# Kernel tuning notes

Hardware: AMD Instinct MI355X
Metric: run time of the kernel (lower is better)

## Reference

```python
import jax, jax.numpy as jnp
import numpy as np

B, S, D, H, DK, DV = 4, 2048, 512, 8, 64, 64
LN_EPS = 1e-5


def setup_inputs() -> dict:
    key = jax.random.key(0)
    ks = jax.random.split(key, 8)
    scale = 1.0 / np.sqrt(D)
    return {
        "input_Q": jax.random.normal(ks[0], (B, S, D), jnp.float32),
        "input_K": jax.random.normal(ks[1], (B, S, D), jnp.float32),
        "input_V": jax.random.normal(ks[2], (B, S, D), jnp.float32),
        "attn_mask": jax.random.randint(ks[3], (B, S, S), 0, 2).astype(jnp.bool_),
        "W_Q": jax.random.normal(ks[4], (D, H * DK), jnp.float32) * scale,
        "W_K": jax.random.normal(ks[5], (D, H * DK), jnp.float32) * scale,
        "W_V": jax.random.normal(ks[6], (D, H * DV), jnp.float32) * scale,
        "W_fc": jax.random.normal(ks[7], (H * DV, D), jnp.float32) * scale,
        "ln_gamma": jnp.ones((D,), jnp.float32),
        "ln_beta": jnp.zeros((D,), jnp.float32),
    }


def reference(input_Q, input_K, input_V, attn_mask, W_Q, W_K, W_V, W_fc, ln_gamma, ln_beta):
    b, s, _ = input_Q.shape
    # projections -> [b, h, s, d]
    Q = (input_Q @ W_Q).reshape(b, s, H, DK).transpose(0, 2, 1, 3)
    K = (input_K @ W_K).reshape(b, s, H, DK).transpose(0, 2, 1, 3)
    V = (input_V @ W_V).reshape(b, s, H, DV).transpose(0, 2, 1, 3)
    # full [b, h, q, k] score matrix (faithful to explicit matmul->mask->softmax)
    scores = jnp.einsum("bhqd,bhkd->bhqk", Q, K) / np.sqrt(DK).astype(np.float32)
    scores = jnp.where(attn_mask[:, None, :, :], -jnp.inf, scores)
    attn = jax.nn.softmax(scores, axis=-1)
    context = jnp.einsum("bhqk,bhkd->bhqd", attn, V)  # [b, h, s, dv]
    context = context.transpose(0, 2, 1, 3).reshape(b, s, H * DV)
    output = context @ W_fc  # dropout is identity in eval / p=0
    x = output + input_Q  # residual
    mean = jnp.mean(x, axis=-1, keepdims=True)
    var = jnp.var(x, axis=-1, keepdims=True)
    return (x - mean) * jax.lax.rsqrt(var + LN_EPS) * ln_gamma + ln_beta
```

## Files before the change

### kernel.cpp

```cpp
#include <hip/hip_runtime.h>


#define B_ 4
#define S_ 2048
#define D_ 512
#define H_ 8

typedef __attribute__((ext_vector_type(8))) short short8_t;
typedef __attribute__((ext_vector_type(4))) short short4_t;
typedef __attribute__((ext_vector_type(4))) float f32x4;
typedef __attribute__((ext_vector_type(16))) float f32x16;
typedef __attribute__((ext_vector_type(4))) unsigned u32x4;
typedef __attribute__((ext_vector_type(2))) unsigned u32x2;

__device__ __forceinline__ short f2bf(float f) {
    unsigned u = __builtin_bit_cast(unsigned, f);
    u += 0x7fff + ((u >> 16) & 1);
    return (short)(u >> 16);
}

__device__ __forceinline__ unsigned pk2(float a, float b) {
    return __builtin_amdgcn_perm(__builtin_bit_cast(unsigned, b),
                                 __builtin_bit_cast(unsigned, a), 0x07060302u);
}

__device__ __forceinline__ float bflo(unsigned u) {
    return __builtin_bit_cast(float, u << 16);
}
__device__ __forceinline__ float bfhi(unsigned u) {
    return __builtin_bit_cast(float, u & 0xffff0000u);
}

__device__ __forceinline__ void gload16(const void* g, void* l) {
    __builtin_amdgcn_global_load_lds(
        (const __attribute__((address_space(1))) unsigned int*)g,
        (__attribute__((address_space(3))) unsigned int*)l, 16, 0, 0);
}

__global__ __launch_bounds__(256) void pack_mask_kernel(const void* __restrict__ mask,
                                                        unsigned* __restrict__ bits) {
    __shared__ int isBool;
    if (threadIdx.x == 0) isBool = 0;
    __syncthreads();
    const unsigned char* bytes = (const unsigned char*)mask;
    if (threadIdx.x < 64) {
        if (bytes[threadIdx.x * 4 + 1] | bytes[threadIdx.x * 4 + 2] | bytes[threadIdx.x * 4 + 3])
            isBool = 1;
    }
    __syncthreads();
    int w = blockIdx.x * 256 + threadIdx.x;
    size_t base = (size_t)w * 32;
    unsigned v = 0;
    if (isBool) {
        const unsigned char* p = bytes + base;
        #pragma unroll
        for (int i = 0; i < 32; ++i) v |= (p[i] ? 1u : 0u) << i;
    } else {
        const int* p = (const int*)mask + base;
        #pragma unroll
        for (int i = 0; i < 32; ++i) v |= (p[i] ? 1u : 0u) << i;
    }
    bits[w] = ~v;
}

__global__ __launch_bounds__(256) void proj_kernel(
    const float* __restrict__ inQ, const float* __restrict__ inK, const float* __restrict__ inV,
    const float* __restrict__ wq, const float* __restrict__ wk, const float* __restrict__ wv,
    short* __restrict__ Qp, short* __restrict__ Kp, short* __restrict__ Vp) {
    __shared__ short As[64 * 64];
    __shared__ short Bs[64 * 64];
    const int z = blockIdx.z;
    const float* A = (z == 0) ? inQ : ((z == 1) ? inK : inV);
    const float* W = (z == 0) ? wq : ((z == 1) ? wk : wv);
    short* O = (z == 0) ? Qp : ((z == 1) ? Kp : Vp);
    const float scale = (z == 0) ? 0.125f * 1.44269504f : 1.0f;
    const int bm = blockIdx.x * 64, bn = blockIdx.y * 64;
    const int tid = threadIdx.x, lane = tid & 63, wv_ = tid >> 6;
    const int wm = (wv_ >> 1) * 32, wn = (wv_ & 1) * 32;
    f32x4 acc[2][2] = {};

    for (int k0 = 0; k0 < 512; k0 += 64) {
        __syncthreads();
        #pragma unroll
        for (int it = 0; it < 4; ++it) {
            int g = tid + it * 256;
            int r = g >> 4, c4 = (g & 15) * 4;
            f32x4 v = *(const f32x4*)(A + (size_t)(bm + r) * 512 + k0 + c4);
            u32x2 u = { pk2(v.x, v.y), pk2(v.z, v.w) };
            *(u32x2*)((char*)As + r * 128 + ((c4 * 2) ^ ((r & 7) << 4))) = u;
        }
        #pragma unroll
        for (int it = 0; it < 2; ++it) {
            int g = tid + it * 256;
            int kp = g >> 4, n4 = (g & 15) * 4;
            const float* wrow = W + (size_t)(k0 + 2 * kp) * 512 + bn + n4;
            f32x4 va = *(const f32x4*)(wrow);
            f32x4 vb = *(const f32x4*)(wrow + 512);
            #pragma unroll
            for (int j = 0; j < 4; ++j) {
                int n = n4 + j;
                *(unsigned*)((char*)Bs + n * 128 + ((4 * kp) ^ ((n & 7) << 4))) = pk2(va[j], vb[j]);
            }
        }
        __syncthreads();
        #pragma unroll
        for (int kk = 0; kk < 2; ++kk) {
            short8_t af[2], bfr[2];
            #pragma unroll
            for (int rf = 0; rf < 2; ++rf) {
                int row = wm + rf * 16 + (lane & 15);
                af[rf] = *(const short8_t*)((const char*)As + row * 128 +
                          ((kk * 64 + ((lane >> 4) * 16)) ^ ((row & 7) << 4)));
            }
            #pragma unroll
            for (int cf = 0; cf < 2; ++cf) {
                int n = wn + cf * 16 + (lane & 15);
                bfr[cf] = *(const short8_t*)((const char*)Bs + n * 128 +
                           ((kk * 64 + ((lane >> 4) * 16)) ^ ((n & 7) << 4)));
            }
            __builtin_amdgcn_s_setprio(1);
            #pragma unroll
            for (int rf = 0; rf < 2; ++rf)
                #pragma unroll
                for (int cf = 0; cf < 2; ++cf)
                    acc[rf][cf] = __builtin_amdgcn_mfma_f32_16x16x32_bf16(af[rf], bfr[cf], acc[rf][cf], 0, 0, 0);
            __builtin_amdgcn_s_setprio(0);
        }
    }
    if (z == 2) {
        #pragma unroll
        for (int rf = 0; rf < 2; ++rf)
            #pragma unroll
            for (int cf = 0; cf < 2; ++cf) {
                int col = bn + wn + cf * 16 + (lane & 15);
                int row0 = bm + wm + rf * 16 + (lane >> 4) * 4;
                int bb = row0 >> 11, ss = row0 & 2047;
                size_t off = ((size_t)(bb * 8 + (col >> 6)) * 64 + (col & 63)) * 2048 + ss;
                short4_t v4 = { f2bf(acc[rf][cf][0]), f2bf(acc[rf][cf][1]),
                                f2bf(acc[rf][cf][2]), f2bf(acc[rf][cf][3]) };
                *(short4_t*)(O + off) = v4;
            }
    } else {
        #pragma unroll
        for (int rf = 0; rf < 2; ++rf)
            #pragma unroll
            for (int cf = 0; cf < 2; ++cf)
                #pragma unroll
                for (int r = 0; r < 4; ++r) {
                    int row = bm + wm + rf * 16 + (lane >> 4) * 4 + r;
                    int col = bn + wn + cf * 16 + (lane & 15);
                    size_t idx = ((((size_t)(row >> 11)) * 8 + (col >> 6)) * 2048 + (row & 2047)) * 64 + (col & 63);
                    O[idx] = f2bf(acc[rf][cf][r] * scale);
                }
    }
}

template<int NSPLIT>
__global__ __launch_bounds__(256, 4) void attn_kernel(
    const short* __restrict__ Qp, const short* __restrict__ Kp, const short* __restrict__ Vt,
    const unsigned long long* __restrict__ mbits64, short* __restrict__ ctx,
    short* __restrict__ pO, float* __restrict__ pL) {
    __shared__ short Ks[2][64 * 64];
    __shared__ short Vts[2][64 * 64];
    const int b = blockIdx.z;
    const int h = (NSPLIT > 1) ? ((int)blockIdx.y / NSPLIT) : blockIdx.y;
    const int kvh = (NSPLIT > 1) ? ((int)blockIdx.y % NSPLIT) : 0;
    const int q_blk = blockIdx.x * 128;
    const int tid = threadIdx.x, lane = tid & 63, w = tid >> 6;
    const int hi = lane >> 5, r31 = lane & 31;
    const size_t hb = ((size_t)(b * 8 + h)) * 131072;
    const int qw = q_blk + w * 32;
    const int q_lane = qw + r31;
    const int NT = 32 / NSPLIT;
    const int t_beg = kvh * NT;
    const int t_end = t_beg + NT;

    short8_t qf[4];
    #pragma unroll
    for (int ks = 0; ks < 4; ++ks)
        qf[ks] = *(const short8_t*)(Qp + hb + (size_t)q_lane * 64 + ks * 16 + hi * 8);

    f32x16 o0 = {}, o1 = {};
    float l_run = 0.f;

    const int sub = lane >> 3, chk = lane & 7;
    const int colsrc = (chk * 16) ^ (sub << 4);
    const int swz = (lane & 7) << 4;

    #pragma unroll
    for (int ii = 0; ii < 2; ++ii) {
        int row = w * 16 + ii * 8 + sub;
        gload16((const char*)(Kp + hb + (size_t)(t_beg * 64 + row) * 64) + colsrc, &Ks[0][(w * 16 + ii * 8) * 64]);
        gload16((const char*)(Vt + hb + (size_t)row * 2048 + t_beg * 64) + colsrc, &Vts[0][(w * 16 + ii * 8) * 64]);
    }
    __syncthreads();

    for (int kt = t_beg; kt < t_end; ++kt) {
        const int buf = (kt - t_beg) & 1;
        const short* Kb = Ks[buf];
        const short* Vb = Vts[buf];
        if (kt < t_end - 1) {
            int nb = buf ^ 1;
            #pragma unroll
            for (int ii = 0; ii < 2; ++ii) {
                int row = w * 16 + ii * 8 + sub;
                gload16((const char*)(Kp + hb + (size_t)((kt + 1) * 64 + row) * 64) + colsrc,
                        &Ks[nb][(w * 16 + ii * 8) * 64]);
                gload16((const char*)(Vt + hb + (size_t)row * 2048 + (kt + 1) * 64) + colsrc,
                        &Vts[nb][(w * 16 + ii * 8) * 64]);
            }
        }
        unsigned long long wmx = mbits64[((size_t)(b * 2048 + q_lane)) * 32 + kt] >> (hi * 4);
        unsigned kl = (unsigned)wmx, kh = (unsigned)(wmx >> 32);

        f32x16 s0 = {}, s1 = {};
        __builtin_amdgcn_s_setprio(1);
        #pragma unroll
        for (int ks = 0; ks < 4; ++ks) {
            short8_t kf0 = *(const short8_t*)((const char*)Kb + (size_t)r31 * 128 + ((ks * 32 + hi * 16) ^ swz));
            short8_t kf1 = *(const short8_t*)((const char*)Kb + (size_t)(32 + r31) * 128 + ((ks * 32 + hi * 16) ^ swz));
            s0 = __builtin_amdgcn_mfma_f32_32x32x16_bf16(kf0, qf[ks], s0, 0, 0, 0);
            s1 = __builtin_amdgcn_mfma_f32_32x32x16_bf16(kf1, qf[ks], s1, 0, 0, 0);
        }
        __builtin_amdgcn_s_setprio(0);

        float r4[4] = { 0.f, 0.f, 0.f, 0.f };
        #pragma unroll
        for (int reg = 0; reg < 16; ++reg) {
            const int pos = (reg >> 2) * 8 + (reg & 3);
            float e0 = __builtin_amdgcn_exp2f(s0[reg]);
            float e1 = __builtin_amdgcn_exp2f(s1[reg]);
            unsigned k0b = (unsigned)__builtin_amdgcn_sbfe((int)kl, pos, 1);
            unsigned k1b = (unsigned)__builtin_amdgcn_sbfe((int)kh, pos, 1);
            float v0 = __builtin_bit_cast(float, __builtin_bit_cast(unsigned, e0) & k0b);
            float v1 = __builtin_bit_cast(float, __builtin_bit_cast(unsigned, e1) & k1b);
            s0[reg] = v0; s1[reg] = v1;
            r4[reg & 3] += v0 + v1;
        }
        float rs = (r4[0] + r4[1]) + (r4[2] + r4[3]);
        rs += __shfl_xor(rs, 32, 64);
        l_run += rs;

        #pragma unroll
        for (int kb = 0; kb < 4; ++kb) {
            const int e = (kb & 1) * 8;
            unsigned c0 = (kb < 2) ? pk2(s0[e + 0], s0[e + 1]) : pk2(s1[e + 0], s1[e + 1]);
            unsigned c1 = (kb < 2) ? pk2(s0[e + 2], s0[e + 3]) : pk2(s1[e + 2], s1[e + 3]);
            unsigned c2 = (kb < 2) ? pk2(s0[e + 4], s0[e + 5]) : pk2(s1[e + 4], s1[e + 5]);
            unsigned c3 = (kb < 2) ? pk2(s0[e + 6], s0[e + 7]) : pk2(s1[e + 6], s1[e + 7]);
#if __has_builtin(__builtin_amdgcn_permlane32_swap)
            u32x2 r02 = __builtin_amdgcn_permlane32_swap(c0, c2, false, false);
            u32x2 r13 = __builtin_amdgcn_permlane32_swap(c1, c3, false, false);
            u32x4 bw = { r02[0], r13[0], r02[1], r13[1] };
#else
            unsigned x0 = __shfl_xor(c0, 32, 64), x1 = __shfl_xor(c1, 32, 64);
            unsigned x2 = __shfl_xor(c2, 32, 64), x3 = __shfl_xor(c3, 32, 64);
            unsigned w0 = hi ? x2 : c0, w1 = hi ? x3 : c1;
            unsigned w2 = hi ? c2 : x0, w3 = hi ? c3 : x1;
            u32x4 bw = { w0, w1, w2, w3 };
#endif
            short8_t pb = __builtin_bit_cast(short8_t, bw);
            short8_t vf0 = *(const short8_t*)((const char*)Vb + (size_t)r31 * 128 + ((kb * 32 + hi * 16) ^ swz));
            short8_t vf1 = *(const short8_t*)((const char*)Vb + (size_t)(32 + r31) * 128 + ((kb * 32 + hi * 16) ^ swz));
            __builtin_amdgcn_s_setprio(1);
            o0 = __builtin_amdgcn_mfma_f32_32x32x16_bf16(vf0, pb, o0, 0, 0, 0);
            o1 = __builtin_amdgcn_mfma_f32_32x32x16_bf16(vf1, pb, o1, 0, 0, 0);
            __builtin_amdgcn_s_setprio(0);
        }
        __syncthreads();
    }

    float invl = 1.0f / fmaxf(l_run, 1e-37f);
    short* Pw = ((short*)Ks) + (size_t)w * 2048;
    #pragma unroll
    for (int dvb = 0; dvb < 2; ++dvb)
        #pragma unroll
        for (int g = 0; g < 4; ++g) {
            short4_t v4;
            #pragma unroll
            for (int t = 0; t < 4; ++t) {
                float val = (dvb ? o1[g * 4 + t] : o0[g * 4 + t]) * invl;
                v4[t] = f2bf(val);
            }
            int dv0 = dvb * 32 + g * 8 + hi * 4;
            *(short4_t*)((char*)Pw + r31 * 128 + ((dv0 * 2) ^ ((r31 & 7) << 4))) = v4;
        }
    asm volatile("s_waitcnt lgkmcnt(0)" ::: "memory");
    if (NSPLIT > 1) {
        const size_t bhn = (size_t)((b * 8 + h) * NSPLIT + kvh);
        #pragma unroll
        for (int c = 0; c < 4; ++c) {
            int idx = c * 64 + lane;
            int qq = idx >> 3, ch = idx & 7;
            short8_t rowv = *(const short8_t*)((const char*)Pw + qq * 128 + ((ch * 16) ^ ((qq & 7) << 4)));
            *(short8_t*)(pO + (bhn * 2048 + qw + qq) * 64 + ch * 8) = rowv;
        }
        if (lane < 32) pL[bhn * 2048 + q_lane] = l_run;
    } else {
        #pragma unroll
        for (int c = 0; c < 4; ++c) {
            int idx = c * 64 + lane;
            int qq = idx >> 3, ch = idx & 7;
            short8_t rowv = *(const short8_t*)((const char*)Pw + qq * 128 + ((ch * 16) ^ ((qq & 7) << 4)));
            *(short8_t*)(ctx + ((size_t)(b * 2048 + qw + qq)) * 512 + h * 64 + ch * 8) = rowv;
        }
    }
}

template<int NSPLIT>
__global__ __launch_bounds__(256) void combine_kernel(
    const short* __restrict__ pO, const float* __restrict__ pL,
    short* __restrict__ ctx) {
    const int row = blockIdx.x;
    const int b = row >> 11, q = row & 2047;
    const int e0 = threadIdx.x * 2;
    const int h = e0 >> 6, dv = e0 & 63;
    const size_t base = ((size_t)((b * 8 + h) * NSPLIT)) * 2048 + q;
    float wsum = 0.f, r0 = 0.f, r1 = 0.f;
    #pragma unroll
    for (int i = 0; i < NSPLIT; ++i) {
        float wv = pL[base + (size_t)i * 2048];
        unsigned a = *(const unsigned*)(pO + (base + (size_t)i * 2048) * 64 + dv);
        wsum += wv;
        r0 += bflo(a) * wv;
        r1 += bfhi(a) * wv;
    }
    float inv = 1.f / fmaxf(wsum, 1e-37f);
    *(unsigned*)(ctx + (size_t)row * 512 + e0) = pk2(r0 * inv, r1 * inv);
}

__global__ __launch_bounds__(256) void fc_kernel(
    const short* __restrict__ ctx, const float* __restrict__ wfc,
    const float* __restrict__ inQ, float* __restrict__ xbuf) {
    __shared__ short As[64 * 64];
    __shared__ short Bs[64 * 64];
    const int bm = blockIdx.x * 64, bn = blockIdx.y * 64;
    const int tid = threadIdx.x, lane = tid & 63, wv_ = tid >> 6;
    const int wm = (wv_ >> 1) * 32, wn = (wv_ & 1) * 32;
    f32x4 acc[2][2] = {};

    for (int k0 = 0; k0 < 512; k0 += 64) {
        __syncthreads();
        #pragma unroll
        for (int it = 0; it < 2; ++it) {
            int g = tid + it * 256;
            int r = g >> 3, c8 = (g & 7) * 8;
            short8_t v = *(const short8_t*)(ctx + (size_t)(bm + r) * 512 + k0 + c8);
            *(short8_t*)((char*)As + r * 128 + ((c8 * 2) ^ ((r & 7) << 4))) = v;
        }
        #pragma unroll
        for (int it = 0; it < 2; ++it) {
            int g = tid + it * 256;
            int kp = g >> 4, n4 = (g & 15) * 4;
            const float* wrow = wfc + (size_t)(k0 + 2 * kp) * 512 + bn + n4;
            f32x4 va = *(const f32x4*)(wrow);
            f32x4 vb = *(const f32x4*)(wrow + 512);
            #pragma unroll
            for (int j = 0; j < 4; ++j) {
                int n = n4 + j;
                *(unsigned*)((char*)Bs + n * 128 + ((4 * kp) ^ ((n & 7) << 4))) = pk2(va[j], vb[j]);
            }
        }
        __syncthreads();
        #pragma unroll
        for (int kk = 0; kk < 2; ++kk) {
            short8_t af[2], bfr[2];
            #pragma unroll
            for (int rf = 0; rf < 2; ++rf) {
                int row = wm + rf * 16 + (lane & 15);
                af[rf] = *(const short8_t*)((const char*)As + row * 128 +
                          ((kk * 64 + ((lane >> 4) * 16)) ^ ((row & 7) << 4)));
            }
            #pragma unroll
            for (int cf = 0; cf < 2; ++cf) {
                int n = wn + cf * 16 + (lane & 15);
                bfr[cf] = *(const short8_t*)((const char*)Bs + n * 128 +
                           ((kk * 64 + ((lane >> 4) * 16)) ^ ((n & 7) << 4)));
            }
            __builtin_amdgcn_s_setprio(1);
            #pragma unroll
            for (int rf = 0; rf < 2; ++rf)
                #pragma unroll
                for (int cf = 0; cf < 2; ++cf)
                    acc[rf][cf] = __builtin_amdgcn_mfma_f32_16x16x32_bf16(af[rf], bfr[cf], acc[rf][cf], 0, 0, 0);
            __builtin_amdgcn_s_setprio(0);
        }
    }
    #pragma unroll
    for (int rf = 0; rf < 2; ++rf)
        #pragma unroll
        for (int cf = 0; cf < 2; ++cf)
            #pragma unroll
            for (int r = 0; r < 4; ++r) {
                int row = bm + wm + rf * 16 + (lane >> 4) * 4 + r;
                int col = bn + wn + cf * 16 + (lane & 15);
                size_t idx = (size_t)row * 512 + col;
                xbuf[idx] = acc[rf][cf][r] + inQ[idx];
            }
}

__global__ __launch_bounds__(256) void ln_kernel(
    const float* __restrict__ x, const float* __restrict__ gamma,
    const float* __restrict__ beta, float* __restrict__ out) {
    __shared__ float rs[4], rq[4];
    const int row = blockIdx.x, tid = threadIdx.x;
    const int w = tid >> 6, lane = tid & 63;
    float2 v = *(const float2*)(x + (size_t)row * 512 + tid * 2);
    float s = v.x + v.y, sq = v.x * v.x + v.y * v.y;
    #pragma unroll
    for (int off = 32; off; off >>= 1) {
        s += __shfl_down(s, off, 64);
        sq += __shfl_down(sq, off, 64);
    }
    if (lane == 0) { rs[w] = s; rq[w] = sq; }
    __syncthreads();
    if (tid == 0) {
        rs[0] = rs[0] + rs[1] + rs[2] + rs[3];
        rq[0] = rq[0] + rq[1] + rq[2] + rq[3];
    }
    __syncthreads();
    float mean = rs[0] * (1.f / 512.f);
    float var = rq[0] * (1.f / 512.f) - mean * mean;
    float inv = rsqrtf(var + 1e-5f);
    int c0 = tid * 2;
    float2 g = *(const float2*)(gamma + c0);
    float2 be = *(const float2*)(beta + c0);
    float2 o;
    o.x = (v.x - mean) * inv * g.x + be.x;
    o.y = (v.y - mean) * inv * g.y + be.y;
    *(float2*)(out + (size_t)row * 512 + c0) = o;
}

extern "C" void kernel_launch(void* const* d_in, const int* in_sizes, int n_in,
                              void* d_out, int out_size, void* d_ws, size_t ws_size,
                              hipStream_t stream) {
    const float* inQ = (const float*)d_in[0];
    const float* inK = (const float*)d_in[1];
    const float* inV = (const float*)d_in[2];
    const void* mask = d_in[3];
    const float* wq = (const float*)d_in[4];
    const float* wk = (const float*)d_in[5];
    const float* wv = (const float*)d_in[6];
    const float* wfc = (const float*)d_in[7];
    const float* gamma = (const float*)d_in[8];
    const float* beta = (const float*)d_in[9];
    float* out = (float*)d_out;
    char* ws = (char*)d_ws;

    short* Qp = (short*)(ws);
    short* Kp = (short*)(ws + (size_t)(8 << 20));
    short* Vp = (short*)(ws + (size_t)(16 << 20));
    short* ctx = (short*)(ws + (size_t)(24 << 20));
    unsigned* mbits = (unsigned*)(ws + (size_t)(32 << 20));
    float* xbuf = (float*)(ws);

    short* pO2 = (short*)(ws + 35651584ull);
    float* pL2 = (float*)(ws + 35651584ull + 16777216ull);
    short* pO4 = (short*)(ws + 35651584ull);
    float* pL4 = (float*)(ws + 35651584ull + 33554432ull);

    const bool split4 = ws_size >= (35651584ull + 33554432ull + 1048576ull);
    const bool split2 = ws_size >= 53477376ull;

    pack_mask_kernel<<<2048, 256, 0, stream>>>(mask, mbits);
    proj_kernel<<<dim3(128, 8, 3), 256, 0, stream>>>(inQ, inK, inV, wq, wk, wv, Qp, Kp, Vp);
    if (split4) {
        attn_kernel<4><<<dim3(16, 32, 4), 256, 0, stream>>>(
            Qp, Kp, Vp, (const unsigned long long*)mbits, ctx, pO4, pL4);
        combine_kernel<4><<<8192, 256, 0, stream>>>(pO4, pL4, ctx);
    } else if (split2) {
        attn_kernel<2><<<dim3(16, 16, 4), 256, 0, stream>>>(
            Qp, Kp, Vp, (const unsigned long long*)mbits, ctx, pO2, pL2);
        combine_kernel<2><<<8192, 256, 0, stream>>>(pO2, pL2, ctx);
    } else {
        attn_kernel<1><<<dim3(16, 8, 4), 256, 0, stream>>>(
            Qp, Kp, Vp, (const unsigned long long*)mbits, ctx, pO2, pL2);
    }
    fc_kernel<<<dim3(128, 8, 1), 256, 0, stream>>>(ctx, wfc, inQ, xbuf);
    ln_kernel<<<8192, 256, 0, stream>>>(xbuf, gamma, beta, out);
}
```

Before: 147.5 us.

## Store K/V in MFMA fragment order and read attention operands directly from global

The projection kernel now writes K and V tiles through LDS into a pre-swizzled, fragment-ordered layout, so the attention kernel can load MFMA operands straight from global/L2 without LDS staging, double buffering or per-tile barriers. The mask bitmap is repacked to be indexed per key tile and query, which makes the per-lane mask loads coalesced. Attention blocks are remapped so that blocks sharing a (batch, head, split) are grouped for L2 locality, and the 4-way KV split is dropped in favour of the 2-way split. This trades LDS reuse across the four waves for redundant global/L2 reads, and adds an extra LDS transpose pass in the projection epilogue.

```diff
diff --git a/kernel.cpp b/kernel.cpp
--- a/kernel.cpp
+++ b/kernel.cpp
@@ -29,12 +29,6 @@
 }
 __device__ __forceinline__ float bfhi(unsigned u) {
     return __builtin_bit_cast(float, u & 0xffff0000u);
-}
-
-__device__ __forceinline__ void gload16(const void* g, void* l) {
-    __builtin_amdgcn_global_load_lds(
-        (const __attribute__((address_space(1))) unsigned int*)g,
-        (__attribute__((address_space(3))) unsigned int*)l, 16, 0, 0);
 }
 
 __global__ __launch_bounds__(256) void pack_mask_kernel(const void* __restrict__ mask,
@@ -48,19 +42,20 @@
             isBool = 1;
     }
     __syncthreads();
-    int w = blockIdx.x * 256 + threadIdx.x;
-    size_t base = (size_t)w * 32;
+    int t = blockIdx.x * 256 + threadIdx.x;
+    int half = t & 1, q = (t >> 1) & 2047, kt = (t >> 12) & 31, b = t >> 17;
+    size_t src = ((size_t)(b * 2048 + q)) * 2048 + kt * 64 + half * 32;
     unsigned v = 0;
     if (isBool) {
-        const unsigned char* p = bytes + base;
+        const unsigned char* p = bytes + src;
         #pragma unroll
         for (int i = 0; i < 32; ++i) v |= (p[i] ? 1u : 0u) << i;
     } else {
-        const int* p = (const int*)mask + base;
+        const int* p = (const int*)mask + src;
         #pragma unroll
         for (int i = 0; i < 32; ++i) v |= (p[i] ? 1u : 0u) << i;
     }
-    bits[w] = ~v;
+    bits[(((size_t)(b * 32 + kt)) * 2048 + q) * 2 + half] = ~v;
 }
 
 __global__ __launch_bounds__(256) void proj_kernel(
@@ -127,20 +122,8 @@
             __builtin_amdgcn_s_setprio(0);
         }
     }
-    if (z == 2) {
-        #pragma unroll
-        for (int rf = 0; rf < 2; ++rf)
-            #pragma unroll
-            for (int cf = 0; cf < 2; ++cf) {
-                int col = bn + wn + cf * 16 + (lane & 15);
-                int row0 = bm + wm + rf * 16 + (lane >> 4) * 4;
-                int bb = row0 >> 11, ss = row0 & 2047;
-                size_t off = ((size_t)(bb * 8 + (col >> 6)) * 64 + (col & 63)) * 2048 + ss;
-                short4_t v4 = { f2bf(acc[rf][cf][0]), f2bf(acc[rf][cf][1]),
-                                f2bf(acc[rf][cf][2]), f2bf(acc[rf][cf][3]) };
-                *(short4_t*)(O + off) = v4;
-            }
-    } else {
+
+    if (z == 0) {
         #pragma unroll
         for (int rf = 0; rf < 2; ++rf)
             #pragma unroll
@@ -152,73 +135,88 @@
                     size_t idx = ((((size_t)(row >> 11)) * 8 + (col >> 6)) * 2048 + (row & 2047)) * 64 + (col & 63);
                     O[idx] = f2bf(acc[rf][cf][r] * scale);
                 }
+    } else {
+        const int bb = bm >> 11, kt = (bm & 2047) >> 6, hh = bn >> 6;
+        const size_t base = ((size_t)(bb * 8 + hh)) * 131072 + (size_t)kt * 4096;
+        __syncthreads();
+        if (z == 1) {
+            #pragma unroll
+            for (int rf = 0; rf < 2; ++rf)
+                #pragma unroll
+                for (int cf = 0; cf < 2; ++cf)
+                    #pragma unroll
+                    for (int r = 0; r < 4; ++r) {
+                        int key = wm + rf * 16 + (lane >> 4) * 4 + r;
+                        int dk = wn + cf * 16 + (lane & 15);
+                        *(short*)((char*)As + key * 128 + ((dk * 2) ^ ((key & 7) << 4))) = f2bf(acc[rf][cf][r]);
+                    }
+        } else {
+            #pragma unroll
+            for (int rf = 0; rf < 2; ++rf)
+                #pragma unroll
+                for (int cf = 0; cf < 2; ++cf)
+                    #pragma unroll
+                    for (int r = 0; r < 4; ++r) {
+                        int key = wm + rf * 16 + (lane >> 4) * 4 + r;
+                        int dv = wn + cf * 16 + (lane & 15);
+                        *(short*)((char*)As + dv * 128 + ((key * 2) ^ ((dv & 7) << 4))) = f2bf(acc[rf][cf][r]);
+                    }
+        }
+        __syncthreads();
+        #pragma unroll
+        for (int it = 0; it < 2; ++it) {
+            int u = tid + it * 256;
+            int blk = u >> 7, h2 = (u >> 6) & 1, rr = u & 63;
+            short8_t v8 = *(const short8_t*)((const char*)As + rr * 128 +
+                           ((blk * 32 + h2 * 16) ^ ((rr & 7) << 4)));
+            *(short8_t*)(O + base + (size_t)u * 8) = v8;
+        }
     }
 }
 
 template<int NSPLIT>
 __global__ __launch_bounds__(256, 4) void attn_kernel(
-    const short* __restrict__ Qp, const short* __restrict__ Kp, const short* __restrict__ Vt,
+    const short* __restrict__ Qp, const short* __restrict__ Kf, const short* __restrict__ Vf,
     const unsigned long long* __restrict__ mbits64, short* __restrict__ ctx,
     short* __restrict__ pO, float* __restrict__ pL) {
-    __shared__ short Ks[2][64 * 64];
-    __shared__ short Vts[2][64 * 64];
-    const int b = blockIdx.z;
-    const int h = (NSPLIT > 1) ? ((int)blockIdx.y / NSPLIT) : blockIdx.y;
-    const int kvh = (NSPLIT > 1) ? ((int)blockIdx.y % NSPLIT) : 0;
-    const int q_blk = blockIdx.x * 128;
+    __shared__ short Pw_all[4][2048];
+    int flat = blockIdx.x + 16 * (blockIdx.y + 8 * NSPLIT * blockIdx.z);
+    int x8 = flat & 7, s = flat >> 3;
+    int group = x8 * (4 * NSPLIT) + (s >> 4);
+    int qi = s & 15;
+    int bh = group / NSPLIT, kvh = group % NSPLIT;
+    const int b = bh >> 3, h = bh & 7;
     const int tid = threadIdx.x, lane = tid & 63, w = tid >> 6;
     const int hi = lane >> 5, r31 = lane & 31;
     const size_t hb = ((size_t)(b * 8 + h)) * 131072;
-    const int qw = q_blk + w * 32;
+    const int qw = qi * 128 + w * 32;
     const int q_lane = qw + r31;
     const int NT = 32 / NSPLIT;
-    const int t_beg = kvh * NT;
-    const int t_end = t_beg + NT;
+    const int t_beg = kvh * NT, t_end = t_beg + NT;
 
     short8_t qf[4];
     #pragma unroll
     for (int ks = 0; ks < 4; ++ks)
         qf[ks] = *(const short8_t*)(Qp + hb + (size_t)q_lane * 64 + ks * 16 + hi * 8);
 
+    const short* Kb_ = Kf + hb + hi * 512 + r31 * 8;
+    const short* Vb_ = Vf + hb + hi * 512 + r31 * 8;
+    const unsigned long long* mrow = mbits64 + (size_t)b * 65536 + q_lane;
+
     f32x16 o0 = {}, o1 = {};
     float l_run = 0.f;
 
-    const int sub = lane >> 3, chk = lane & 7;
-    const int colsrc = (chk * 16) ^ (sub << 4);
-    const int swz = (lane & 7) << 4;
-
-    #pragma unroll
-    for (int ii = 0; ii < 2; ++ii) {
-        int row = w * 16 + ii * 8 + sub;
-        gload16((const char*)(Kp + hb + (size_t)(t_beg * 64 + row) * 64) + colsrc, &Ks[0][(w * 16 + ii * 8) * 64]);
-        gload16((const char*)(Vt + hb + (size_t)row * 2048 + t_beg * 64) + colsrc, &Vts[0][(w * 16 + ii * 8) * 64]);
-    }
-    __syncthreads();
-
     for (int kt = t_beg; kt < t_end; ++kt) {
-        const int buf = (kt - t_beg) & 1;
-        const short* Kb = Ks[buf];
-        const short* Vb = Vts[buf];
-        if (kt < t_end - 1) {
-            int nb = buf ^ 1;
-            #pragma unroll
-            for (int ii = 0; ii < 2; ++ii) {
-                int row = w * 16 + ii * 8 + sub;
-                gload16((const char*)(Kp + hb + (size_t)((kt + 1) * 64 + row) * 64) + colsrc,
-                        &Ks[nb][(w * 16 + ii * 8) * 64]);
-                gload16((const char*)(Vt + hb + (size_t)row * 2048 + (kt + 1) * 64) + colsrc,
-                        &Vts[nb][(w * 16 + ii * 8) * 64]);
-            }
-        }
-        unsigned long long wmx = mbits64[((size_t)(b * 2048 + q_lane)) * 32 + kt] >> (hi * 4);
+        const short* kp = Kb_ + (size_t)kt * 4096;
+        unsigned long long wmx = mrow[(size_t)kt * 2048] >> (hi * 4);
         unsigned kl = (unsigned)wmx, kh = (unsigned)(wmx >> 32);
 
         f32x16 s0 = {}, s1 = {};
         __builtin_amdgcn_s_setprio(1);
         #pragma unroll
         for (int ks = 0; ks < 4; ++ks) {
-            short8_t kf0 = *(const short8_t*)((const char*)Kb + (size_t)r31 * 128 + ((ks * 32 + hi * 16) ^ swz));
-            short8_t kf1 = *(const short8_t*)((const char*)Kb + (size_t)(32 + r31) * 128 + ((ks * 32 + hi * 16) ^ swz));
+            short8_t kf0 = *(const short8_t*)(kp + ks * 1024);
+            short8_t kf1 = *(const short8_t*)(kp + ks * 1024 + 256);
             s0 = __builtin_amdgcn_mfma_f32_32x32x16_bf16(kf0, qf[ks], s0, 0, 0, 0);
             s1 = __builtin_amdgcn_mfma_f32_32x32x16_bf16(kf1, qf[ks], s1, 0, 0, 0);
         }
@@ -241,6 +239,7 @@
         rs += __shfl_xor(rs, 32, 64);
         l_run += rs;
 
+        const short* vp = Vb_ + (size_t)kt * 4096;
         #pragma unroll
         for (int kb = 0; kb < 4; ++kb) {
             const int e = (kb & 1) * 8;
@@ -260,18 +259,17 @@
             u32x4 bw = { w0, w1, w2, w3 };
 #endif
             short8_t pb = __builtin_bit_cast(short8_t, bw);
-            short8_t vf0 = *(const short8_t*)((const char*)Vb + (size_t)r31 * 128 + ((kb * 32 + hi * 16) ^ swz));
-            short8_t vf1 = *(const short8_t*)((const char*)Vb + (size_t)(32 + r31) * 128 + ((kb * 32 + hi * 16) ^ swz));
+            short8_t vf0 = *(const short8_t*)(vp + kb * 1024);
+            short8_t vf1 = *(const short8_t*)(vp + kb * 1024 + 256);
             __builtin_amdgcn_s_setprio(1);
             o0 = __builtin_amdgcn_mfma_f32_32x32x16_bf16(vf0, pb, o0, 0, 0, 0);
             o1 = __builtin_amdgcn_mfma_f32_32x32x16_bf16(vf1, pb, o1, 0, 0, 0);
             __builtin_amdgcn_s_setprio(0);
         }
-        __syncthreads();
     }
 
     float invl = 1.0f / fmaxf(l_run, 1e-37f);
-    short* Pw = ((short*)Ks) + (size_t)w * 2048;
+    short* Pw = Pw_all[w];
     #pragma unroll
     for (int dvb = 0; dvb < 2; ++dvb)
         #pragma unroll
@@ -287,7 +285,7 @@
         }
     asm volatile("s_waitcnt lgkmcnt(0)" ::: "memory");
     if (NSPLIT > 1) {
-        const size_t bhn = (size_t)((b * 8 + h) * NSPLIT + kvh);
+        const size_t bhn = (size_t)(bh * NSPLIT + kvh);
         #pragma unroll
         for (int c = 0; c < 4; ++c) {
             int idx = c * 64 + lane;
@@ -454,27 +452,20 @@
     unsigned* mbits = (unsigned*)(ws + (size_t)(32 << 20));
     float* xbuf = (float*)(ws);
 
-    short* pO2 = (short*)(ws + 35651584ull);
-    float* pL2 = (float*)(ws + 35651584ull + 16777216ull);
-    short* pO4 = (short*)(ws + 35651584ull);
-    float* pL4 = (float*)(ws + 35651584ull + 33554432ull);
-
-    const bool split4 = ws_size >= (35651584ull + 33554432ull + 1048576ull);
+    short* pO = (short*)(ws + 35651584ull);
+    float* pL = (float*)(ws + 35651584ull + 16777216ull);
+
     const bool split2 = ws_size >= 53477376ull;
 
     pack_mask_kernel<<<2048, 256, 0, stream>>>(mask, mbits);
     proj_kernel<<<dim3(128, 8, 3), 256, 0, stream>>>(inQ, inK, inV, wq, wk, wv, Qp, Kp, Vp);
-    if (split4) {
-        attn_kernel<4><<<dim3(16, 32, 4), 256, 0, stream>>>(
-            Qp, Kp, Vp, (const unsigned long long*)mbits, ctx, pO4, pL4);
-        combine_kernel<4><<<8192, 256, 0, stream>>>(pO4, pL4, ctx);
-    } else if (split2) {
+    if (split2) {
         attn_kernel<2><<<dim3(16, 16, 4), 256, 0, stream>>>(
-            Qp, Kp, Vp, (const unsigned long long*)mbits, ctx, pO2, pL2);
-        combine_kernel<2><<<8192, 256, 0, stream>>>(pO2, pL2, ctx);
+            Qp, Kp, Vp, (const unsigned long long*)mbits, ctx, pO, pL);
+        combine_kernel<2><<<8192, 256, 0, stream>>>(pO, pL, ctx);
     } else {
         attn_kernel<1><<<dim3(16, 8, 4), 256, 0, stream>>>(
-            Qp, Kp, Vp, (const unsigned long long*)mbits, ctx, pO2, pL2);
+            Qp, Kp, Vp, (const unsigned long long*)mbits, ctx, pO, pL);
     }
     fc_kernel<<<dim3(128, 8, 1), 256, 0, stream>>>(ctx, wfc, inQ, xbuf);
     ln_kernel<<<8192, 256, 0, stream>>>(xbuf, gamma, beta, out);
```

Measured after the change: 142.8 us. 1.03x faster.
